# Optimization experiments

Hardware: AMD Instinct MI355X
Metric: run time of the kernel (lower is better)

## Reference

```python
import jax, jax.numpy as jnp
import numpy as np
from jax import lax

B, T, D_IN, H, L = 256, 160, 40, 768, 3
SCALE = 0.05

def setup_inputs() -> dict:
    key = jax.random.key(0)
    ks = jax.random.split(key, 1 + 3 * L)
    inp = {"x": jax.random.normal(ks[0], (B, T, D_IN), dtype=jnp.float32)}
    in_dims = [D_IN, H, H]
    for l in range(L):
        inp[f"Wi{l}"] = jax.random.normal(ks[1 + 3 * l], (in_dims[l], 4 * H), dtype=jnp.float32) * SCALE
        inp[f"Wh{l}"] = jax.random.normal(ks[2 + 3 * l], (H, 4 * H), dtype=jnp.float32) * SCALE
        inp[f"b{l}"] = jnp.zeros((4 * H,), dtype=jnp.float32)
    return inp

def _lstm_layer(x, Wi, Wh, b):
    # x: [B, T, D]; returns [B, T, H]
    batch = x.shape[0]
    h_dim = Wh.shape[0]
    # Precompute input projections for all timesteps (big GEMM, compute-friendly)
    xw = jnp.einsum('btd,dh->bth', x, Wi) + b  # [B, T, 4H]
    c0 = jnp.zeros((batch, h_dim), dtype=x.dtype)
    h0 = jnp.zeros((batch, h_dim), dtype=x.dtype)

    def step(carry, xw_t):
        c, h = carry
        z = xw_t + h @ Wh  # [B, 4H]
        i, f, g, o = jnp.split(z, 4, axis=-1)  # flax LSTMCell gate order
        i = jax.nn.sigmoid(i)
        f = jax.nn.sigmoid(f)
        g = jnp.tanh(g)
        o = jax.nn.sigmoid(o)
        c_new = f * c + i * g
        h_new = o * jnp.tanh(c_new)
        return (c_new, h_new), h_new

    _, ys = lax.scan(step, (c0, h0), jnp.swapaxes(xw, 0, 1))  # ys: [T, B, H]
    return jnp.swapaxes(ys, 0, 1)

def reference(x, Wi0, Wh0, b0, Wi1, Wh1, b1, Wi2, Wh2, b2):
    h = _lstm_layer(x, Wi0, Wh0, b0)
    h = _lstm_layer(h, Wi1, Wh1, b1)
    h = _lstm_layer(h, Wi2, Wh2, b2)
    # frame_aggregation_mean = True -> mean over time
    return jnp.mean(h, axis=1)
```

## Files before the change

kernel.cpp:

```cpp
#include <hip/hip_runtime.h>
#include <stdint.h>

#define B_   256
#define T_   160
#define DIN_ 40
#define H_   768
#define NG_  3072
#define KP0_ 1024
#define KP12_ 1536
#define XC_  48

typedef _Float16 f16;
typedef _Float16 half8 __attribute__((ext_vector_type(8)));
typedef float f32x4 __attribute__((ext_vector_type(4)));

#define AS1C(p) ((const __attribute__((address_space(1))) uint32_t*)(p))
#define AS3(p)  ((__attribute__((address_space(3))) uint32_t*)(p))

struct Params {
  const f16* wt0; const f16* wt1; const f16* wt2;
  const float* bq; const f16* x16;
  f16* hs0; f16* hs1; f16* hs2;
  const f16* zpad; unsigned* cnt; unsigned* claim; float* out;
};

__device__ __forceinline__ float sigmoid_f(float x) { return 1.f / (1.f + __expf(-x)); }
__device__ __forceinline__ float tanh_f(float x) {
  x = fminf(15.f, fmaxf(-15.f, x));
  float e = __expf(2.f * x);
  return (e - 1.f) / (e + 1.f);
}

__global__ void conv_w(const float* __restrict__ Wi, const float* __restrict__ Wh,
                       int in_dim, int hoff, int Kp, f16* __restrict__ dst) {
  __shared__ f16 tile[64][66];
  const int k0 = blockIdx.x * 64;
  const int by = blockIdx.y;
  const int g = by / 12, j0 = (by % 12) * 64;
  const int tid = threadIdx.x;
  #pragma unroll
  for (int it = 0; it < 16; ++it) {
    int idx = it * 256 + tid;
    int jj = idx & 63;
    int kk = idx >> 6;
    int k = k0 + kk;
    int oc = g * H_ + j0 + jj;
    float v = 0.f;
    if (k < in_dim) v = Wi[(size_t)k * NG_ + oc];
    else if (k >= hoff && k < hoff + H_) v = Wh[(size_t)(k - hoff) * NG_ + oc];
    tile[kk][jj] = (f16)v;
  }
  __syncthreads();
  #pragma unroll
  for (int it = 0; it < 16; ++it) {
    int idx = it * 256 + tid;
    int kk = idx & 63;
    int jj = idx >> 6;
    int np = 4 * (j0 + jj) + g;
    dst[(size_t)np * Kp + k0 + kk] = tile[kk][jj];
  }
}

__global__ void conv_b(const float* __restrict__ b0, const float* __restrict__ b1,
                       const float* __restrict__ b2, float* __restrict__ bq) {
  int id = blockIdx.x * 256 + threadIdx.x;
  if (id < 3 * NG_) {
    int l = id / NG_, np = id % NG_;
    int j = np >> 2, g = np & 3;
    const float* s = (l == 0) ? b0 : (l == 1 ? b1 : b2);
    bq[id] = s[g * H_ + j];
  }
}

__global__ void conv_x(const float* __restrict__ x, f16* __restrict__ x16) {
  int id = blockIdx.x * 256 + threadIdx.x;
  if (id >= T_ * B_ * XC_) return;
  int k = id % XC_;
  int b = (id / XC_) % B_;
  int t = id / (XC_ * B_);
  float v = (k < DIN_) ? x[(size_t)b * (T_ * DIN_) + t * DIN_ + k] : 0.f;
  x16[id] = (f16)v;
}

template<int L>
__device__ __forceinline__ void run_layer(
    const f16* __restrict__ WT, const f16* __restrict__ hin, f16* __restrict__ hown,
    const float* __restrict__ bql, const f16* __restrict__ zpad, float* __restrict__ out,
    unsigned* flg, unsigned& iter, f16* Abuf, float* zred, float* bqs,
    int tid, int lane, int w, int kw, int cw, int btile, int ntile, int n0) {
  constexpr int KP  = (L == 0) ? KP0_ : KP12_;
  constexpr int KQ  = KP / 4;
  constexpr int NKT = KQ / 32;
  constexpr int CH  = (L == 0) ? 128 : 96;

  if (tid < 96) bqs[tid] = bql[tid];

  half8 breg[3 * NKT];
  #pragma unroll
  for (int ct = 0; ct < 3; ++ct) {
    #pragma unroll
    for (int kt = 0; kt < NKT; ++kt) {
      int col = n0 + cw * 48 + ct * 16 + (lane & 15);
      int k = kw * KQ + kt * 32 + (lane >> 4) * 8;
      breg[ct * NKT + kt] = *(const half8*)(WT + (size_t)col * KP + k);
    }
  }

  auto stage_hin = [&](int slot) {
    #pragma unroll
    for (int i = 0; i < 24; ++i) {
      int cb = (w - 6) * 1536 + i * 64;
      int idx = cb + lane;
      int row = idx / 96;
      int c = idx - row * 96;
      int cg = c ^ (row & 7);
      int b = btile * 32 + row;
      const f16* src = hin + ((size_t)slot * B_ + b) * H_ + cg * 8;
      __builtin_amdgcn_global_load_lds(AS1C(src), AS3(Abuf + (size_t)cb * 8), 16, 0, 0);
    }
  };
  if (L > 0 && tid >= 384) stage_hin(1);

  const int id = tid;
  const int grow = id / 12, gjp = id - grow * 12;
  const int gb = btile * 32 + grow;
  const int ghc0 = ntile * 24 + 2 * gjp;
  float c0 = 0.f, c1 = 0.f, oa0 = 0.f, oa1 = 0.f;

  for (int t = 0; t < T_; ++t) {
    if (L == 0) {
      #pragma unroll
      for (int i = 0; i < 8; ++i) {
        int cb = w * 512 + i * 64;
        int idx = cb + lane;
        int row = idx >> 7;
        int c = idx & 127;
        int cg = c ^ (row & 7);
        int b = btile * 32 + row;
        const f16* src;
        if (cg < 6)        src = hin + ((size_t)t * B_ + b) * XC_ + cg * 8;
        else if (cg < 102) src = hown + ((size_t)t * B_ + b) * H_ + (cg - 6) * 8;
        else               src = zpad;
        __builtin_amdgcn_global_load_lds(AS1C(src), AS3(Abuf + (size_t)cb * 8), 16, 0, 0);
      }
    } else if (w >= 4) {
      #pragma unroll
      for (int i = 0; i < 12; ++i) {
        int cb = (w - 4) * 768 + i * 64;
        int idx = cb + lane;
        int row = idx / 96;
        int c = idx - row * 96;
        int cg = c ^ (row & 7);
        int b = btile * 32 + row;
        const f16* src = hown + ((size_t)t * B_ + b) * H_ + cg * 8;
        __builtin_amdgcn_global_load_lds(AS1C(src), AS3(Abuf + (size_t)(32 * 768 + cb * 8)), 16, 0, 0);
      }
    }
    asm volatile("s_waitcnt vmcnt(0)" ::: "memory");
    __syncthreads();

    f32x4 acc[2][3] = {};
    const char* Ab = (const char*)(Abuf + (L == 0 ? 0 : (kw >> 1) * 32 * 768));
    const int cbase = (L == 0) ? kw * 32 : (kw & 1) * 48;
    #pragma unroll
    for (int kt = 0; kt < NKT; ++kt) {
      int c = cbase + kt * 4 + (lane >> 4);
      int row0 = (lane & 15);
      half8 a0 = *(const half8*)(Ab + (size_t)row0 * (CH * 16) + (size_t)(c ^ (row0 & 7)) * 16);
      int row1 = 16 + (lane & 15);
      half8 a1 = *(const half8*)(Ab + (size_t)row1 * (CH * 16) + (size_t)(c ^ (row1 & 7)) * 16);
      #pragma unroll
      for (int ct = 0; ct < 3; ++ct) {
        acc[0][ct] = __builtin_amdgcn_mfma_f32_16x16x32_f16(a0, breg[ct * NKT + kt], acc[0][ct], 0, 0, 0);
        acc[1][ct] = __builtin_amdgcn_mfma_f32_16x16x32_f16(a1, breg[ct * NKT + kt], acc[1][ct], 0, 0, 0);
      }
    }

    {
      float* zr = zred + kw * 3072;
      #pragma unroll
      for (int rt = 0; rt < 2; ++rt) {
        #pragma unroll
        for (int ct = 0; ct < 3; ++ct) {
          int row = rt * 16 + (lane >> 4) * 4;
          int col = cw * 48 + ct * 16 + (lane & 15);
          #pragma unroll
          for (int r4 = 0; r4 < 4; ++r4)
            zr[(size_t)(row + r4) * 96 + col] = acc[rt][ct][r4];
        }
      }
    }
    __syncthreads();

    if (tid >= 384) {
      if (L > 0 && t + 1 < T_) stage_hin(t + 2);
    } else {
      const float* z = zred + (size_t)id * 8;
      f32x4 za = *(const f32x4*)(z)        + *(const f32x4*)(z + 3072)
               + *(const f32x4*)(z + 6144) + *(const f32x4*)(z + 9216);
      f32x4 zb = *(const f32x4*)(z + 4)        + *(const f32x4*)(z + 3076)
               + *(const f32x4*)(z + 6148)     + *(const f32x4*)(z + 9220);
      za += *(const f32x4*)(bqs + gjp * 8);
      zb += *(const f32x4*)(bqs + gjp * 8 + 4);
      float i0 = sigmoid_f(za[0]), f0 = sigmoid_f(za[1]), g0 = tanh_f(za[2]), o0 = sigmoid_f(za[3]);
      float i1 = sigmoid_f(zb[0]), f1 = sigmoid_f(zb[1]), g1 = tanh_f(zb[2]), o1 = sigmoid_f(zb[3]);
      float cn0 = f0 * c0 + i0 * g0;
      float cn1 = f1 * c1 + i1 * g1;
      c0 = cn0; c1 = cn1;
      float h0 = o0 * tanh_f(cn0);
      float h1 = o1 * tanh_f(cn1);
      f16 hh0 = (f16)h0, hh1 = (f16)h1;
      unsigned u = ((unsigned)__builtin_bit_cast(uint16_t, hh1) << 16)
                 |  (unsigned)__builtin_bit_cast(uint16_t, hh0);
      unsigned* hp = (unsigned*)(hown + ((size_t)(t + 1) * B_ + gb) * H_ + ghc0);
      __hip_atomic_store(hp, u, __ATOMIC_RELAXED, __HIP_MEMORY_SCOPE_WORKGROUP);
      if (L == 2) {
        oa0 += h0; oa1 += h1;
        if (t == T_ - 1) {
          out[(size_t)gb * H_ + ghc0]     = oa0 * (1.f / T_);
          out[(size_t)gb * H_ + ghc0 + 1] = oa1 * (1.f / T_);
        }
      }
    }

    if (tid < 384) { asm volatile("s_waitcnt vmcnt(0)" ::: "memory"); }
    __syncthreads();
    ++iter;
    if (w == 5) {
      if (lane == 0)
        __hip_atomic_store(flg + (size_t)ntile * 32, iter,
                           __ATOMIC_RELAXED, __HIP_MEMORY_SCOPE_AGENT);
      unsigned* fp = flg + (size_t)(lane & 31) * 32;
      for (;;) {
        unsigned v = __hip_atomic_load(fp, __ATOMIC_RELAXED, __HIP_MEMORY_SCOPE_AGENT);
        if (__ballot(v >= iter) == ~0ull) break;
        __builtin_amdgcn_s_sleep(1);
      }
    }
    __syncthreads();
  }
}

__global__ __launch_bounds__(512, 2) void lstm_main(Params p) {
  __shared__ __align__(16) f16 Abuf[2 * 32 * 768];
  __shared__ __align__(16) float zred[4 * 32 * 96];
  __shared__ __align__(16) float bqs[96];
  __shared__ unsigned claim_s[2];

  const int tid = threadIdx.x;
  const int lane = tid & 63;
  const int w = tid >> 6;
  const int kw = w >> 1, cw = w & 1;

  if (tid == 0) {
    unsigned xcc;
    asm volatile("s_getreg_b32 %0, hwreg(HW_REG_XCC_ID)" : "=s"(xcc));
    xcc &= 7u;
    unsigned slot = __hip_atomic_fetch_add(p.claim + xcc, 1u,
                                           __ATOMIC_RELAXED, __HIP_MEMORY_SCOPE_AGENT);
    claim_s[0] = xcc;
    claim_s[1] = slot & 31u;
  }
  __syncthreads();
  const int btile = (int)claim_s[0];
  const int ntile = (int)claim_s[1];
  unsigned* flg = p.cnt + (size_t)btile * 1024;
  const int n0 = ntile * 96;
  unsigned iter = 0;

  run_layer<0>(p.wt0, p.x16, p.hs0, p.bq + 0 * NG_ + n0, p.zpad, p.out, flg, iter,
               Abuf, zred, bqs, tid, lane, w, kw, cw, btile, ntile, n0);
  run_layer<1>(p.wt1, p.hs0, p.hs1, p.bq + 1 * NG_ + n0, p.zpad, p.out, flg, iter,
               Abuf, zred, bqs, tid, lane, w, kw, cw, btile, ntile, n0);
  run_layer<2>(p.wt2, p.hs1, p.hs2, p.bq + 2 * NG_ + n0, p.zpad, p.out, flg, iter,
               Abuf, zred, bqs, tid, lane, w, kw, cw, btile, ntile, n0);
}

extern "C" void kernel_launch(void* const* d_in, const int* in_sizes, int n_in,
                              void* d_out, int out_size, void* d_ws, size_t ws_size,
                              hipStream_t stream) {
  const float* x   = (const float*)d_in[0];
  const float* Wi0 = (const float*)d_in[1];
  const float* Wh0 = (const float*)d_in[2];
  const float* b0  = (const float*)d_in[3];
  const float* Wi1 = (const float*)d_in[4];
  const float* Wh1 = (const float*)d_in[5];
  const float* b1  = (const float*)d_in[6];
  const float* Wi2 = (const float*)d_in[7];
  const float* Wh2 = (const float*)d_in[8];
  const float* b2  = (const float*)d_in[9];

  char* wsb = (char*)d_ws;
  size_t off = 0;
  auto nxt = [&](size_t sz) { char* p = wsb + off; off += (sz + 255) & ~(size_t)255; return p; };
  f16*      wt0  = (f16*)nxt((size_t)NG_ * KP0_ * 2);
  f16*      wt1  = (f16*)nxt((size_t)NG_ * KP12_ * 2);
  f16*      wt2  = (f16*)nxt((size_t)NG_ * KP12_ * 2);
  float*    bq   = (float*)nxt((size_t)3 * NG_ * 4);
  f16*      x16  = (f16*)nxt((size_t)T_ * B_ * XC_ * 2);
  f16*      hs0  = (f16*)nxt((size_t)(T_ + 1) * B_ * H_ * 2);
  f16*      hs1  = (f16*)nxt((size_t)(T_ + 1) * B_ * H_ * 2);
  f16*      hs2  = (f16*)nxt((size_t)(T_ + 1) * B_ * H_ * 2);
  f16*      zpad = (f16*)nxt(256);
  unsigned* cnt  = (unsigned*)nxt(8 * 1024 * 4);
  unsigned* claim= (unsigned*)nxt(256);
  if (off > ws_size) return;

  const size_t slot_bytes = (size_t)B_ * H_ * 2;
  hipMemsetAsync(hs0, 0, slot_bytes, stream);
  hipMemsetAsync(hs1, 0, slot_bytes, stream);
  hipMemsetAsync(hs2, 0, slot_bytes, stream);
  hipMemsetAsync((void*)zpad, 0, 256, stream);
  hipMemsetAsync(cnt, 0, 8 * 1024 * 4, stream);
  hipMemsetAsync(claim, 0, 256, stream);

  hipLaunchKernelGGL(conv_w, dim3(KP0_ / 64, 48), dim3(256), 0, stream, Wi0, Wh0, DIN_, XC_, KP0_, wt0);
  hipLaunchKernelGGL(conv_w, dim3(KP12_ / 64, 48), dim3(256), 0, stream, Wi1, Wh1, H_, H_, KP12_, wt1);
  hipLaunchKernelGGL(conv_w, dim3(KP12_ / 64, 48), dim3(256), 0, stream, Wi2, Wh2, H_, H_, KP12_, wt2);
  hipLaunchKernelGGL(conv_b, dim3((3 * NG_ + 255) / 256), dim3(256), 0, stream, b0, b1, b2, bq);
  hipLaunchKernelGGL(conv_x, dim3((T_ * B_ * XC_ + 255) / 256), dim3(256), 0, stream, x, x16);

  Params prm{wt0, wt1, wt2, bq, x16, hs0, hs1, hs2, zpad, cnt, claim, (float*)d_out};
  hipLaunchKernelGGL(lstm_main, dim3(256), dim3(512), 0, stream, prm);
}
```

Baseline: 5.973 ms.

## Read recurrent state from a small ring buffer and add fast-path sync flags

```diff
diff --git a/kernel.cpp b/kernel.cpp
--- a/kernel.cpp
+++ b/kernel.cpp
@@ -9,6 +9,9 @@
 #define KP0_ 1024
 #define KP12_ 1536
 #define XC_  48
+#define RS_  16
+#define FR_  64
+#define BH_  ((size_t)B_ * H_)
 
 typedef _Float16 f16;
 typedef _Float16 half8 __attribute__((ext_vector_type(8)));
@@ -20,8 +23,9 @@
 struct Params {
   const f16* wt0; const f16* wt1; const f16* wt2;
   const float* bq; const f16* x16;
-  f16* hs0; f16* hs1; f16* hs2;
-  const f16* zpad; unsigned* cnt; unsigned* claim; float* out;
+  f16* hs0; f16* hs1;
+  f16* ring;
+  const f16* zpad; unsigned* cnt; unsigned* flgW; unsigned* claim; float* out;
 };
 
 __device__ __forceinline__ float sigmoid_f(float x) { return 1.f / (1.f + __expf(-x)); }
@@ -85,8 +89,9 @@
 template<int L>
 __device__ __forceinline__ void run_layer(
     const f16* __restrict__ WT, const f16* __restrict__ hin, f16* __restrict__ hown,
+    f16* __restrict__ hring,
     const float* __restrict__ bql, const f16* __restrict__ zpad, float* __restrict__ out,
-    unsigned* flg, unsigned& iter, f16* Abuf, float* zred, float* bqs,
+    unsigned* flg, unsigned* flgW, unsigned& iter, f16* Abuf, float* zred, float* bqs,
     int tid, int lane, int w, int kw, int cw, int btile, int ntile, int n0) {
   constexpr int KP  = (L == 0) ? KP0_ : KP12_;
   constexpr int KQ  = KP / 4;
@@ -128,6 +133,7 @@
   float c0 = 0.f, c1 = 0.f, oa0 = 0.f, oa1 = 0.f;
 
   for (int t = 0; t < T_; ++t) {
+    const int rslot = t & (RS_ - 1);
     if (L == 0) {
       #pragma unroll
       for (int i = 0; i < 8; ++i) {
@@ -139,7 +145,7 @@
         int b = btile * 32 + row;
         const f16* src;
         if (cg < 6)        src = hin + ((size_t)t * B_ + b) * XC_ + cg * 8;
-        else if (cg < 102) src = hown + ((size_t)t * B_ + b) * H_ + (cg - 6) * 8;
+        else if (cg < 102) src = hring + ((size_t)rslot * B_ + b) * H_ + (cg - 6) * 8;
         else               src = zpad;
         __builtin_amdgcn_global_load_lds(AS1C(src), AS3(Abuf + (size_t)cb * 8), 16, 0, 0);
       }
@@ -152,7 +158,7 @@
         int c = idx - row * 96;
         int cg = c ^ (row & 7);
         int b = btile * 32 + row;
-        const f16* src = hown + ((size_t)t * B_ + b) * H_ + cg * 8;
+        const f16* src = hring + ((size_t)rslot * B_ + b) * H_ + cg * 8;
         __builtin_amdgcn_global_load_lds(AS1C(src), AS3(Abuf + (size_t)(32 * 768 + cb * 8)), 16, 0, 0);
       }
     }
@@ -212,9 +218,12 @@
       f16 hh0 = (f16)h0, hh1 = (f16)h1;
       unsigned u = ((unsigned)__builtin_bit_cast(uint16_t, hh1) << 16)
                  |  (unsigned)__builtin_bit_cast(uint16_t, hh0);
-      unsigned* hp = (unsigned*)(hown + ((size_t)(t + 1) * B_ + gb) * H_ + ghc0);
-      __hip_atomic_store(hp, u, __ATOMIC_RELAXED, __HIP_MEMORY_SCOPE_WORKGROUP);
-      if (L == 2) {
+      unsigned* rp = (unsigned*)(hring + ((size_t)((t + 1) & (RS_ - 1)) * B_ + gb) * H_ + ghc0);
+      __hip_atomic_store(rp, u, __ATOMIC_RELAXED, __HIP_MEMORY_SCOPE_WORKGROUP);
+      if (L < 2) {
+        unsigned* hp = (unsigned*)(hown + ((size_t)(t + 1) * B_ + gb) * H_ + ghc0);
+        __hip_atomic_store(hp, u, __ATOMIC_RELAXED, __HIP_MEMORY_SCOPE_WORKGROUP);
+      } else {
         oa0 += h0; oa1 += h1;
         if (t == T_ - 1) {
           out[(size_t)gb * H_ + ghc0]     = oa0 * (1.f / T_);
@@ -227,14 +236,22 @@
     __syncthreads();
     ++iter;
     if (w == 5) {
-      if (lane == 0)
+      if (lane == 0) {
+        __hip_atomic_store(flgW + ((size_t)(iter & (FR_ - 1)) * 32 + ntile) * 32, iter,
+                           __ATOMIC_RELAXED, __HIP_MEMORY_SCOPE_WORKGROUP);
         __hip_atomic_store(flg + (size_t)ntile * 32, iter,
                            __ATOMIC_RELAXED, __HIP_MEMORY_SCOPE_AGENT);
-      unsigned* fp = flg + (size_t)(lane & 31) * 32;
-      for (;;) {
-        unsigned v = __hip_atomic_load(fp, __ATOMIC_RELAXED, __HIP_MEMORY_SCOPE_AGENT);
-        if (__ballot(v >= iter) == ~0ull) break;
-        __builtin_amdgcn_s_sleep(1);
+      }
+      volatile const unsigned* fw =
+          flgW + ((size_t)(iter & (FR_ - 1)) * 32 + (lane & 31)) * 32;
+      unsigned v = *fw;
+      if (__ballot(v >= iter) != ~0ull) {
+        unsigned* fp = flg + (size_t)(lane & 31) * 32;
+        for (;;) {
+          v = __hip_atomic_load(fp, __ATOMIC_RELAXED, __HIP_MEMORY_SCOPE_AGENT);
+          if (__ballot(v >= iter) == ~0ull) break;
+          __builtin_amdgcn_s_sleep(1);
+        }
       }
     }
     __syncthreads();
@@ -264,15 +281,20 @@
   __syncthreads();
   const int btile = (int)claim_s[0];
   const int ntile = (int)claim_s[1];
-  unsigned* flg = p.cnt + (size_t)btile * 1024;
+  unsigned* flg  = p.cnt  + (size_t)btile * 1024;
+  unsigned* flgW = p.flgW + (size_t)btile * (FR_ * 32 * 32);
   const int n0 = ntile * 96;
   unsigned iter = 0;
 
-  run_layer<0>(p.wt0, p.x16, p.hs0, p.bq + 0 * NG_ + n0, p.zpad, p.out, flg, iter,
+  f16* ring0 = p.ring;
+  f16* ring1 = p.ring + (size_t)RS_ * BH_;
+  f16* ring2 = p.ring + (size_t)2 * RS_ * BH_;
+
+  run_layer<0>(p.wt0, p.x16, p.hs0, ring0, p.bq + 0 * NG_ + n0, p.zpad, p.out, flg, flgW, iter,
                Abuf, zred, bqs, tid, lane, w, kw, cw, btile, ntile, n0);
-  run_layer<1>(p.wt1, p.hs0, p.hs1, p.bq + 1 * NG_ + n0, p.zpad, p.out, flg, iter,
+  run_layer<1>(p.wt1, p.hs0, p.hs1, ring1, p.bq + 1 * NG_ + n0, p.zpad, p.out, flg, flgW, iter,
                Abuf, zred, bqs, tid, lane, w, kw, cw, btile, ntile, n0);
-  run_layer<2>(p.wt2, p.hs1, p.hs2, p.bq + 2 * NG_ + n0, p.zpad, p.out, flg, iter,
+  run_layer<2>(p.wt2, p.hs1, (f16*)nullptr, ring2, p.bq + 2 * NG_ + n0, p.zpad, p.out, flg, flgW, iter,
                Abuf, zred, bqs, tid, lane, w, kw, cw, btile, ntile, n0);
 }
 
@@ -298,20 +320,23 @@
   f16*      wt2  = (f16*)nxt((size_t)NG_ * KP12_ * 2);
   float*    bq   = (float*)nxt((size_t)3 * NG_ * 4);
   f16*      x16  = (f16*)nxt((size_t)T_ * B_ * XC_ * 2);
-  f16*      hs0  = (f16*)nxt((size_t)(T_ + 1) * B_ * H_ * 2);
-  f16*      hs1  = (f16*)nxt((size_t)(T_ + 1) * B_ * H_ * 2);
-  f16*      hs2  = (f16*)nxt((size_t)(T_ + 1) * B_ * H_ * 2);
+  f16*      hs0  = (f16*)nxt((size_t)(T_ + 1) * BH_ * 2);
+  f16*      hs1  = (f16*)nxt((size_t)(T_ + 1) * BH_ * 2);
+  f16*      ring = (f16*)nxt((size_t)3 * RS_ * BH_ * 2);
   f16*      zpad = (f16*)nxt(256);
   unsigned* cnt  = (unsigned*)nxt(8 * 1024 * 4);
+  unsigned* flgW = (unsigned*)nxt((size_t)8 * FR_ * 32 * 128);
   unsigned* claim= (unsigned*)nxt(256);
   if (off > ws_size) return;
 
-  const size_t slot_bytes = (size_t)B_ * H_ * 2;
-  hipMemsetAsync(hs0, 0, slot_bytes, stream);
-  hipMemsetAsync(hs1, 0, slot_bytes, stream);
-  hipMemsetAsync(hs2, 0, slot_bytes, stream);
+  hipMemsetAsync(ring, 0, BH_ * 2, stream);
+  hipMemsetAsync(ring + (size_t)RS_ * BH_, 0, BH_ * 2, stream);
+  hipMemsetAsync(ring + (size_t)2 * RS_ * BH_, 0, BH_ * 2, stream);
+  hipMemsetAsync(hs0, 0, BH_ * 2, stream);
+  hipMemsetAsync(hs1, 0, BH_ * 2, stream);
   hipMemsetAsync((void*)zpad, 0, 256, stream);
   hipMemsetAsync(cnt, 0, 8 * 1024 * 4, stream);
+  hipMemsetAsync(flgW, 0, (size_t)8 * FR_ * 32 * 128, stream);
   hipMemsetAsync(claim, 0, 256, stream);
 
   hipLaunchKernelGGL(conv_w, dim3(KP0_ / 64, 48), dim3(256), 0, stream, Wi0, Wh0, DIN_, XC_, KP0_, wt0);
@@ -320,6 +345,6 @@
   hipLaunchKernelGGL(conv_b, dim3((3 * NG_ + 255) / 256), dim3(256), 0, stream, b0, b1, b2, bq);
   hipLaunchKernelGGL(conv_x, dim3((T_ * B_ * XC_ + 255) / 256), dim3(256), 0, stream, x, x16);
 
-  Params prm{wt0, wt1, wt2, bq, x16, hs0, hs1, hs2, zpad, cnt, claim, (float*)d_out};
+  Params prm{wt0, wt1, wt2, bq, x16, hs0, hs1, ring, zpad, cnt, flgW, claim, (float*)d_out};
   hipLaunchKernelGGL(lstm_main, dim3(256), dim3(512), 0, stream, prm);
 }
```

New measurement: 5.569 ms. -6.8%, faster.
